# Performance work log

Hardware: AMD Instinct MI355X
Metric: run time of the kernel (lower is better)

Reference implementation:

```python
import jax, jax.numpy as jnp
import numpy as np

PATCH = 16
STRIDE = 8  # patch_size - overlap

def setup_inputs() -> dict:
    key = jax.random.key(0)
    x = jax.random.normal(key, (16, 3, 512, 512), dtype=jnp.float32)
    return {"x": x, "k_neighbors": 8}

def reference(x, k_neighbors):
    B, C, H, W = x.shape
    p, s = PATCH, STRIDE
    nh = (H - p) // s + 1
    nw = (W - p) // s + 1
    N = nh * nw
    # F.unfold equivalent: feature dim ordered (C, kh, kw), then transpose(1,2)
    patches = jax.lax.conv_general_dilated_patches(
        x, filter_shape=(p, p), window_strides=(s, s), padding='VALID')  # [B, C*p*p, nh, nw]
    patches = patches.reshape(B, C * p * p, N).transpose(0, 2, 1)  # [B, N, C*p*p]
    # grid positions [(i, j)] row-major, same order as the python double loop
    ii, jj = jnp.meshgrid(jnp.arange(nh), jnp.arange(nw), indexing='ij')
    pos = jnp.stack([ii.ravel(), jj.ravel()], axis=1).astype(jnp.float32)  # [N, 2]
    positions = jnp.broadcast_to(pos[None], (B, N, 2))
    k = min(int(k_neighbors) + 1, N)
    def knn(posb):
        # squared euclidean distance preserves the ordering of cdist(p=2)
        d2 = jnp.sum((posb[:, None, :] - posb[None, :, :]) ** 2, axis=-1)  # [N, N]
        _, idx = jax.lax.top_k(-d2, k)  # k smallest distances
        tgt = idx[:, 1:]  # drop self (distance 0)
        src = jnp.broadcast_to(jnp.arange(N)[:, None], tgt.shape)
        return jnp.stack([src.ravel(), tgt.ravel()], axis=0)  # [2, N*k_neighbors]
    edge_index = jax.vmap(knn)(positions)  # [B, 2, N*k_neighbors]
    return patches, positions, edge_index
```

## Files before the change

### kernel.cpp

```cpp
#include <hip/hip_runtime.h>

#define BB     16
#define CH     3
#define HH     512
#define WW     512
#define PATCH_ 16
#define STRIDE_ 8
#define NH     63
#define NW     63
#define NN     3969
#define FDIM   768
#define EDGES  31752

#define PATCHES_ELEMS  (BB * NN * FDIM)
#define POS_ELEMS      (BB * NN * 2)
#define F4             (FDIM / 4)
#define TOTAL_G        (BB * NN * F4)

__global__ __launch_bounds__(256) void patches_kernel(const float* __restrict__ x,
                                                      float* __restrict__ out) {
    unsigned g = blockIdx.x * 256u + threadIdx.x;
    unsigned f4   = g % F4;
    unsigned rest = g / F4;
    unsigned n    = rest % NN;
    unsigned b    = rest / NN;

    unsigned f  = f4 << 2;
    unsigned c  = f >> 8;
    unsigned di = (f >> 4) & 15;
    unsigned dj = f & 15;
    unsigned i  = n / NW;
    unsigned j  = n - i * NW;
    unsigned row = i * STRIDE_ + di;
    unsigned col = j * STRIDE_ + dj;

    const float4 v = *reinterpret_cast<const float4*>(
        x + ((size_t)((b * CH + c) * HH + row) * WW + col));
    *reinterpret_cast<float4*>(out + (size_t)g * 4) = v;
}

__global__ __launch_bounds__(256) void pos_kernel(float* __restrict__ out) {
    unsigned g = blockIdx.x * 256u + threadIdx.x;
    if (g >= BB * NN) return;
    unsigned n = g % NN;
    unsigned i = n / NW;
    unsigned j = n - i * NW;
    *reinterpret_cast<float2*>(out + (size_t)g * 2) =
        make_float2((float)i, (float)j);
}

__global__ __launch_bounds__(256) void edge_kernel(float* __restrict__ out) {
    unsigned n = blockIdx.x * 256u + threadIdx.x;
    if (n >= NN) return;
    int i = (int)(n / NW);
    int j = (int)(n - i * NW);

    unsigned best[9];
#pragma unroll
    for (int s = 0; s < 9; ++s) best[s] = 0xFFFFFFFFu;

    for (int di = -2; di <= 2; ++di) {
        int ni = i + di;
        if (ni < 0 || ni >= NH) continue;
        for (int dj = -2; dj <= 2; ++dj) {
            int nj = j + dj;
            if (nj < 0 || nj >= NW) continue;
            unsigned d2  = (unsigned)(di * di + dj * dj);
            unsigned key = (d2 << 12) | (unsigned)(ni * NW + nj);
#pragma unroll
            for (int s = 0; s < 9; ++s) {
                if (key < best[s]) { unsigned t = best[s]; best[s] = key; key = t; }
            }
        }
    }

    float tg[8];
#pragma unroll
    for (int t = 0; t < 8; ++t) tg[t] = (float)(best[t + 1] & 0xFFFu);

    float  src = (float)n;
    float4 s4  = make_float4(src, src, src, src);
    float4 t0  = make_float4(tg[0], tg[1], tg[2], tg[3]);
    float4 t1  = make_float4(tg[4], tg[5], tg[6], tg[7]);

    for (int b = 0; b < BB; ++b) {
        float* base = out + (size_t)b * 2 * EDGES;
        *reinterpret_cast<float4*>(base + (size_t)n * 8)         = s4;
        *reinterpret_cast<float4*>(base + (size_t)n * 8 + 4)     = s4;
        *reinterpret_cast<float4*>(base + EDGES + (size_t)n * 8)     = t0;
        *reinterpret_cast<float4*>(base + EDGES + (size_t)n * 8 + 4) = t1;
    }
}

extern "C" void kernel_launch(void* const* d_in, const int* in_sizes, int n_in,
                              void* d_out, int out_size, void* d_ws, size_t ws_size,
                              hipStream_t stream) {
    const float* x = (const float*)d_in[0];
    float* out     = (float*)d_out;

    float* patches = out;
    float* pos     = out + PATCHES_ELEMS;
    float* edge    = out + PATCHES_ELEMS + POS_ELEMS;

    patches_kernel<<<TOTAL_G / 256, 256, 0, stream>>>(x, patches);
    pos_kernel<<<(BB * NN + 255) / 256, 256, 0, stream>>>(pos);
    edge_kernel<<<(NN + 255) / 256, 256, 0, stream>>>(edge);
}
```

Measured before the change: 252.3 us.

## Fuse patch, position and edge kernels into one launch with nontemporal stores

Merges the three kernels into a single launch whose blocks are split by block index: patch-copy blocks first, then blocks that write positions and edges. Each patch thread now copies a full 16-float row (four vector loads) instead of one float4, and all output writes use nontemporal stores. Edge work is spread over batch×N threads instead of looping over batch per thread. This removes two launches and their serialization, and cuts per-thread index arithmetic, at the cost of fewer threads for the patch copy and possibly less cache reuse of the overlapping input rows.

```diff
diff --git a/kernel.cpp b/kernel.cpp
--- a/kernel.cpp
+++ b/kernel.cpp
@@ -1,94 +1,96 @@
 #include <hip/hip_runtime.h>
 
-#define BB     16
-#define CH     3
-#define HH     512
-#define WW     512
-#define PATCH_ 16
-#define STRIDE_ 8
-#define NH     63
-#define NW     63
-#define NN     3969
-#define FDIM   768
-#define EDGES  31752
+#define BB      16
+#define CH      3
+#define HH      512
+#define WW      512
+#define NH      63
+#define NW      63
+#define NN      3969
+#define FDIM    768
+#define EDGES   31752
 
 #define PATCHES_ELEMS  (BB * NN * FDIM)
 #define POS_ELEMS      (BB * NN * 2)
-#define F4             (FDIM / 4)
-#define TOTAL_G        (BB * NN * F4)
 
-__global__ __launch_bounds__(256) void patches_kernel(const float* __restrict__ x,
-                                                      float* __restrict__ out) {
-    unsigned g = blockIdx.x * 256u + threadIdx.x;
-    unsigned f4   = g % F4;
-    unsigned rest = g / F4;
-    unsigned n    = rest % NN;
-    unsigned b    = rest / NN;
+#define F16            (FDIM / 16)
+#define PATCH_THREADS  (BB * NN * F16)
+#define PATCH_BLOCKS   (PATCH_THREADS / 256)
+#define PE_THREADS     (BB * NN)
+#define PE_BLOCKS      ((PE_THREADS + 255) / 256)
 
-    unsigned f  = f4 << 2;
-    unsigned c  = f >> 8;
-    unsigned di = (f >> 4) & 15;
-    unsigned dj = f & 15;
-    unsigned i  = n / NW;
-    unsigned j  = n - i * NW;
-    unsigned row = i * STRIDE_ + di;
-    unsigned col = j * STRIDE_ + dj;
+typedef float  f4 __attribute__((ext_vector_type(4)));
+typedef float  f2 __attribute__((ext_vector_type(2)));
 
-    const float4 v = *reinterpret_cast<const float4*>(
-        x + ((size_t)((b * CH + c) * HH + row) * WW + col));
-    *reinterpret_cast<float4*>(out + (size_t)g * 4) = v;
-}
+__global__ __launch_bounds__(256) void fused_kernel(const float* __restrict__ x,
+                                                    float* __restrict__ out) {
+    unsigned bid = blockIdx.x;
 
-__global__ __launch_bounds__(256) void pos_kernel(float* __restrict__ out) {
-    unsigned g = blockIdx.x * 256u + threadIdx.x;
-    if (g >= BB * NN) return;
-    unsigned n = g % NN;
-    unsigned i = n / NW;
-    unsigned j = n - i * NW;
-    *reinterpret_cast<float2*>(out + (size_t)g * 2) =
-        make_float2((float)i, (float)j);
-}
+    if (bid < PATCH_BLOCKS) {
+        unsigned t    = bid * 256u + threadIdx.x;
+        unsigned f16  = t % F16;
+        unsigned rest = t / F16;
+        unsigned n    = rest % NN;
+        unsigned b    = rest / NN;
+        unsigned c    = f16 >> 4;
+        unsigned di   = f16 & 15;
+        unsigned i    = n / NW;
+        unsigned j    = n - i * NW;
 
-__global__ __launch_bounds__(256) void edge_kernel(float* __restrict__ out) {
-    unsigned n = blockIdx.x * 256u + threadIdx.x;
-    if (n >= NN) return;
-    int i = (int)(n / NW);
-    int j = (int)(n - i * NW);
+        const float* src = x + ((size_t)((b * CH + c) * HH + i * 8u + di) * WW + j * 8u);
+        f4 v0 = *reinterpret_cast<const f4*>(src + 0);
+        f4 v1 = *reinterpret_cast<const f4*>(src + 4);
+        f4 v2 = *reinterpret_cast<const f4*>(src + 8);
+        f4 v3 = *reinterpret_cast<const f4*>(src + 12);
 
-    unsigned best[9];
+        float* dst = out + (size_t)t * 16;
+        __builtin_nontemporal_store(v0, reinterpret_cast<f4*>(dst + 0));
+        __builtin_nontemporal_store(v1, reinterpret_cast<f4*>(dst + 4));
+        __builtin_nontemporal_store(v2, reinterpret_cast<f4*>(dst + 8));
+        __builtin_nontemporal_store(v3, reinterpret_cast<f4*>(dst + 12));
+    } else {
+        unsigned g = (bid - PATCH_BLOCKS) * 256u + threadIdx.x;
+        if (g >= PE_THREADS) return;
+        unsigned n = g % NN;
+        unsigned b = g / NN;
+        int i = (int)(n / NW);
+        int j = (int)(n - (unsigned)i * NW);
+
+        f2 p; p.x = (float)i; p.y = (float)j;
+        __builtin_nontemporal_store(
+            p, reinterpret_cast<f2*>(out + PATCHES_ELEMS + (size_t)(b * NN + n) * 2));
+
+        unsigned best[9];
 #pragma unroll
-    for (int s = 0; s < 9; ++s) best[s] = 0xFFFFFFFFu;
-
-    for (int di = -2; di <= 2; ++di) {
-        int ni = i + di;
-        if (ni < 0 || ni >= NH) continue;
-        for (int dj = -2; dj <= 2; ++dj) {
-            int nj = j + dj;
-            if (nj < 0 || nj >= NW) continue;
-            unsigned d2  = (unsigned)(di * di + dj * dj);
-            unsigned key = (d2 << 12) | (unsigned)(ni * NW + nj);
+        for (int s = 0; s < 9; ++s) best[s] = 0xFFFFFFFFu;
+        for (int di = -2; di <= 2; ++di) {
+            int ni = i + di;
+            if (ni < 0 || ni >= NH) continue;
+            for (int dj = -2; dj <= 2; ++dj) {
+                int nj = j + dj;
+                if (nj < 0 || nj >= NW) continue;
+                unsigned key = ((unsigned)(di * di + dj * dj) << 12)
+                             | (unsigned)(ni * NW + nj);
 #pragma unroll
-            for (int s = 0; s < 9; ++s) {
-                if (key < best[s]) { unsigned t = best[s]; best[s] = key; key = t; }
+                for (int s = 0; s < 9; ++s) {
+                    if (key < best[s]) { unsigned tmp = best[s]; best[s] = key; key = tmp; }
+                }
             }
         }
-    }
 
-    float tg[8];
-#pragma unroll
-    for (int t = 0; t < 8; ++t) tg[t] = (float)(best[t + 1] & 0xFFFu);
+        float src_f = (float)n;
+        f4 s4; s4.x = src_f; s4.y = src_f; s4.z = src_f; s4.w = src_f;
+        f4 t0, t1;
+        t0.x = (float)(best[1] & 0xFFFu); t0.y = (float)(best[2] & 0xFFFu);
+        t0.z = (float)(best[3] & 0xFFFu); t0.w = (float)(best[4] & 0xFFFu);
+        t1.x = (float)(best[5] & 0xFFFu); t1.y = (float)(best[6] & 0xFFFu);
+        t1.z = (float)(best[7] & 0xFFFu); t1.w = (float)(best[8] & 0xFFFu);
 
-    float  src = (float)n;
-    float4 s4  = make_float4(src, src, src, src);
-    float4 t0  = make_float4(tg[0], tg[1], tg[2], tg[3]);
-    float4 t1  = make_float4(tg[4], tg[5], tg[6], tg[7]);
-
-    for (int b = 0; b < BB; ++b) {
-        float* base = out + (size_t)b * 2 * EDGES;
-        *reinterpret_cast<float4*>(base + (size_t)n * 8)         = s4;
-        *reinterpret_cast<float4*>(base + (size_t)n * 8 + 4)     = s4;
-        *reinterpret_cast<float4*>(base + EDGES + (size_t)n * 8)     = t0;
-        *reinterpret_cast<float4*>(base + EDGES + (size_t)n * 8 + 4) = t1;
+        float* ebase = out + PATCHES_ELEMS + POS_ELEMS + (size_t)b * 2 * EDGES;
+        __builtin_nontemporal_store(s4, reinterpret_cast<f4*>(ebase + (size_t)n * 8));
+        __builtin_nontemporal_store(s4, reinterpret_cast<f4*>(ebase + (size_t)n * 8 + 4));
+        __builtin_nontemporal_store(t0, reinterpret_cast<f4*>(ebase + EDGES + (size_t)n * 8));
+        __builtin_nontemporal_store(t1, reinterpret_cast<f4*>(ebase + EDGES + (size_t)n * 8 + 4));
     }
 }
 
@@ -97,12 +99,5 @@
                               hipStream_t stream) {
     const float* x = (const float*)d_in[0];
     float* out     = (float*)d_out;
-
-    float* patches = out;
-    float* pos     = out + PATCHES_ELEMS;
-    float* edge    = out + PATCHES_ELEMS + POS_ELEMS;
-
-    patches_kernel<<<TOTAL_G / 256, 256, 0, stream>>>(x, patches);
-    pos_kernel<<<(BB * NN + 255) / 256, 256, 0, stream>>>(pos);
-    edge_kernel<<<(NN + 255) / 256, 256, 0, stream>>>(edge);
+    fused_kernel<<<PATCH_BLOCKS + PE_BLOCKS, 256, 0, stream>>>(x, out);
 }
```

Result: slower. 455.4 us (+80.5%).
